# Optimization experiments

Hardware: AMD Instinct MI355X
Metric: run time of the kernel (lower is better)

The kernel has to match this reference:

```python
import jax, jax.numpy as jnp
import numpy as np

B, IN, H, Z = 2048, 1024, 1024, 256


def setup_inputs() -> dict:
    key = jax.random.key(0)
    ks = jax.random.split(key, 17)
    s = 1.0 / np.sqrt(H)  # matches reset_parameters uniform(-stdv, stdv)
    u = lambda k, shape: jax.random.uniform(k, shape, minval=-s, maxval=s, dtype=jnp.float32)
    return {
        'src_x': jax.random.normal(ks[0], (B, IN), dtype=jnp.float32),
        'h': jax.random.normal(ks[1], (B, H), dtype=jnp.float32),
        'c': jax.random.normal(ks[2], (B, H), dtype=jnp.float32),
        'src_meta': jax.random.normal(ks[3], (B, Z), dtype=jnp.float32),
        'zh_w': u(ks[4], (4 * Z, Z)),
        'zh_b': u(ks[5], (4 * Z,)),
        'zx_w': u(ks[6], (4 * Z, Z)),
        'zx_b': u(ks[7], (4 * Z,)),
        'zb_w': u(ks[8], (4 * Z, Z)),
        'dh_w': u(ks[9], (4, H, Z)),
        'dx_w': u(ks[10], (4, H, Z)),
        'db_w': u(ks[11], (4, H, Z)),
        'db_b': u(ks[12], (4, H)),
        'w_h': u(ks[13], (4, H, H)),
        'w_x': u(ks[14], (4, H, IN)),
        'ln_w': u(ks[15], (4, H)),
        'ln_b': u(ks[16], (4, H)),
    }


def reference(src_x, h, c, src_meta, zh_w, zh_b, zx_w, zx_b, zb_w,
              dh_w, dx_w, db_w, db_b, w_h, w_x, ln_w, ln_b):
    b = src_x.shape[0]
    # hypernetwork projections, reshaped to [B, 4 gates, Z]
    zh = (src_meta @ zh_w.T + zh_b).reshape(b, 4, -1)
    zx = (src_meta @ zx_w.T + zx_b).reshape(b, 4, -1)
    zb = (src_meta @ zb_w.T).reshape(b, 4, -1)
    # per-gate scaling vectors d_h, d_x and bias d_b: [B, 4, H]
    d_h = jnp.einsum('bgz,ghz->bgh', zh, dh_w)
    d_x = jnp.einsum('bgz,ghz->bgh', zx, dx_w)
    d_b = jnp.einsum('bgz,ghz->bgh', zb, db_w) + db_b[None]
    # main LSTM matmuls: [B, 4, H]
    wh = jnp.einsum('ghj,bj->bgh', w_h, h)
    wx = jnp.einsum('ghj,bj->bgh', w_x, src_x)
    y = d_h * wh + d_x * wx + d_b
    # per-gate LayerNorm over hidden dim (eps = 1e-5, torch default)
    mu = jnp.mean(y, axis=-1, keepdims=True)
    var = jnp.var(y, axis=-1, keepdims=True)
    yn = (y - mu) * jax.lax.rsqrt(var + 1e-5) * ln_w[None] + ln_b[None]
    i, f, g, o = yn[:, 0], yn[:, 1], yn[:, 2], yn[:, 3]
    c_next = jax.nn.sigmoid(f) * c + jax.nn.sigmoid(i) * jnp.tanh(g)
    h_next = jax.nn.sigmoid(o) * jnp.tanh(c_next)
    return (h_next, c_next)
```

## Files before the change

### kernel.cpp

```cpp
#include <hip/hip_runtime.h>

typedef __attribute__((ext_vector_type(4))) float f32x4;
typedef __attribute__((ext_vector_type(8))) short bf16x8;

#define DEVFN static __device__ __forceinline__

DEVFN unsigned short f2bf(float f) {
  union { float f; unsigned u; } x; x.f = f;
  unsigned r = x.u + 0x7fffu + ((x.u >> 16) & 1u);
  return (unsigned short)(r >> 16);
}
DEVFN float bf2f(unsigned short u) {
  union { unsigned u; float f; } x; x.u = ((unsigned)u) << 16;
  return x.f;
}

DEVFN void gload_lds16(const unsigned short* g, unsigned short* l) {
  __builtin_amdgcn_global_load_lds(
      (const __attribute__((address_space(1))) unsigned int*)g,
      (__attribute__((address_space(3))) unsigned int*)l, 16, 0, 0);
}

#define NSEG 8
struct SegTable {
  const float* src[NSEG];
  unsigned short* dst[NSEG];
  int chunks[NSEG];
};

__global__ __launch_bounds__(256) void prep_kernel(
    SegTable st, int castChunks,
    const float* __restrict__ zh_w, const float* __restrict__ zx_w,
    const float* __restrict__ zb_w, unsigned short* __restrict__ WzT,
    const float* __restrict__ zh_b, const float* __restrict__ zx_b,
    const float* __restrict__ db_b, const float* __restrict__ dh_w,
    const float* __restrict__ dx_w, float* __restrict__ F) {
  __shared__ float T[64][65];
  const int tid = threadIdx.x;
  int b = blockIdx.x;

  if (b < castChunks) {
    int c = b, s = 0;
    while (c >= st.chunks[s]) { c -= st.chunks[s]; ++s; }
    const float* src = st.src[s] + (long)c * 4096;
    unsigned short* dst = st.dst[s] + (long)c * 4096;
#pragma unroll
    for (int i = 0; i < 4; ++i) {
      float4 v = *(const float4*)(src + tid * 4 + i * 1024);
      ushort4 o;
      o.x = f2bf(v.x); o.y = f2bf(v.y); o.z = f2bf(v.z); o.w = f2bf(v.w);
      *(ushort4*)(dst + tid * 4 + i * 1024) = o;
    }
    return;
  }
  b -= castChunks;

  if (b < 192) {
    const int zz = b >> 4, rem = b & 15;
    const int t = zz >> 2, g = zz & 3;
    const float* src =
        (t == 0 ? zh_w : (t == 1 ? zx_w : zb_w)) + (long)g * 65536;
    unsigned short* dst = WzT + (long)zz * 65536;
    const int j0 = (rem & 3) * 64, k0 = (rem >> 2) * 64;
    const int jr = tid >> 2, kc = (tid & 3) * 16;
#pragma unroll
    for (int i = 0; i < 4; ++i) {
      float4 v = *(const float4*)(src + (long)(j0 + jr) * 256 + k0 + kc + i * 4);
      T[jr][kc + i * 4 + 0] = v.x;
      T[jr][kc + i * 4 + 1] = v.y;
      T[jr][kc + i * 4 + 2] = v.z;
      T[jr][kc + i * 4 + 3] = v.w;
    }
    __syncthreads();
    const int kr = tid >> 2, jc = (tid & 3) * 16;
    unsigned short tmp[16];
#pragma unroll
    for (int i = 0; i < 16; ++i) tmp[i] = f2bf(T[jc + i][kr]);
    *(bf16x8*)(dst + (long)(k0 + kr) * 256 + j0 + jc) = *(bf16x8*)&tmp[0];
    *(bf16x8*)(dst + (long)(k0 + kr) * 256 + j0 + jc + 8) = *(bf16x8*)&tmp[8];
    return;
  }
  b -= 192;

  if (b >= 128) {
    const int idx = (b - 128) * 1024 + tid * 4;
    *(float4*)(F + 8192 + idx) = *(const float4*)(db_b + idx);
    return;
  }
  const int wgid = b * 4 + (tid >> 6);
  const int lane = tid & 63;
  const int t = wgid >> 8, g = (wgid >> 6) & 3, hbase = (wgid & 63) * 16;
  const float* zb = (t == 0 ? zh_b : zx_b) + g * 256;
  const float* dw = (t == 0 ? dh_w : dx_w) + (long)g * 262144;
  float4 zv = *(const float4*)(zb + lane * 4);
#pragma unroll
  for (int i = 0; i < 16; ++i) {
    const int h = hbase + i;
    float4 wv = *(const float4*)(dw + (long)h * 256 + lane * 4);
    float s = zv.x * wv.x + zv.y * wv.y + zv.z * wv.z + zv.w * wv.w;
#pragma unroll
    for (int off = 32; off; off >>= 1) s += __shfl_down(s, off);
    if (lane == 0) F[(t * 4 + g) * 1024 + h] = s;
  }
}

DEVFN void gemm128_body(const unsigned short* __restrict__ A,
                        const unsigned short* __restrict__ W,
                        unsigned short* __restrict__ C,
                        const float* __restrict__ bias,
                        int lda, int ldb, int ldc, int K,
                        int bx, int by,
                        unsigned short* As, unsigned short* Bs) {
  const int m0 = by * 128, n0 = bx * 128;
  const int tid = threadIdx.x;
  const int lane = tid & 63, wid = tid >> 6;
  const int wr = wid >> 1, wc = wid & 1;

  const int srow = tid >> 2, scol = (tid & 3) * 8;
  const unsigned short* Ag0 = A + (long)(m0 + srow) * lda + scol;
  const unsigned short* Ag1 = A + (long)(m0 + 64 + srow) * lda + scol;
  const unsigned short* Wg0 = W + (long)(n0 + srow) * ldb + scol;
  const unsigned short* Wg1 = W + (long)(n0 + 64 + srow) * ldb + scol;
  unsigned short* As0 = &As[tid * 8];
  unsigned short* As1 = &As[2048 + tid * 8];
  unsigned short* Bs0 = &Bs[tid * 8];
  unsigned short* Bs1 = &Bs[2048 + tid * 8];

  const int r = lane & 15, q = lane >> 4;

  f32x4 acc[4][4];
#pragma unroll
  for (int m = 0; m < 4; ++m)
#pragma unroll
    for (int n = 0; n < 4; ++n) acc[m][n] = (f32x4)0.f;

  for (int k0 = 0; k0 < K; k0 += 32) {
    gload_lds16(Ag0 + k0, As0);
    gload_lds16(Ag1 + k0, As1);
    gload_lds16(Wg0 + k0, Bs0);
    gload_lds16(Wg1 + k0, Bs1);
    __syncthreads();

    bf16x8 af[4], bfr[4];
#pragma unroll
    for (int m = 0; m < 4; ++m)
      af[m] = *(const bf16x8*)&As[(wr * 64 + m * 16 + r) * 32 + q * 8];
#pragma unroll
    for (int n = 0; n < 4; ++n)
      bfr[n] = *(const bf16x8*)&Bs[(wc * 64 + n * 16 + r) * 32 + q * 8];
#pragma unroll
    for (int m = 0; m < 4; ++m)
#pragma unroll
      for (int n = 0; n < 4; ++n)
        acc[m][n] = __builtin_amdgcn_mfma_f32_16x16x32_bf16(af[m], bfr[n],
                                                            acc[m][n], 0, 0, 0);
    __syncthreads();
  }

#pragma unroll
  for (int m = 0; m < 4; ++m) {
    const int row = m0 + wr * 64 + m * 16 + q * 4;
#pragma unroll
    for (int n = 0; n < 4; ++n) {
      const int col = n0 + wc * 64 + n * 16 + r;
      float bv = bias ? bias[col] : 0.f;
#pragma unroll
      for (int j = 0; j < 4; ++j) {
        float v = acc[m][n][j] + bv;
        C[(long)(row + j) * ldc + col] = f2bf(v);
      }
    }
  }
}

__global__ __launch_bounds__(256) void gemm_e(
    const unsigned short* __restrict__ Wd, const unsigned short* __restrict__ WzT,
    unsigned short* __restrict__ E) {
  __shared__ __align__(16) unsigned short As[4096];
  __shared__ __align__(16) unsigned short Bs[4096];
  const int zz = blockIdx.z;
  gemm128_body(Wd + (long)zz * 262144, WzT + (long)zz * 65536,
               E + (long)zz * 262144, nullptr,
               256, 256, 256, 256, blockIdx.x, blockIdx.y, As, Bs);
}

__global__ __launch_bounds__(256) void gemm_d(
    const unsigned short* __restrict__ meta_bf, const unsigned short* __restrict__ E,
    unsigned short* __restrict__ dall, const float* __restrict__ F) {
  __shared__ __align__(16) unsigned short As[4096];
  __shared__ __align__(16) unsigned short Bs[4096];
  const int zz = blockIdx.z;
  unsigned short* C = dall + (long)(zz >> 2) * 8388608 + (zz & 3) * 1024;
  gemm128_body(meta_bf, E + (long)zz * 262144, C, F + zz * 1024,
               256, 256, 4096, 256, blockIdx.x, blockIdx.y, As, Bs);
}

__global__ __launch_bounds__(512, 2) void gemm256_whx(
    const unsigned short* __restrict__ Aall,
    const unsigned short* __restrict__ Ball,
    unsigned short* __restrict__ Call) {
  __shared__ __align__(16) unsigned short As[2][2][8192];
  __shared__ __align__(16) unsigned short Bs[2][2][8192];

  const int bid = blockIdx.x;
  const int swz = (bid & 7) * 32 + (bid >> 3);
  const int z = swz >> 7;
  const int rr = swz & 127;
  const int sb = rr >> 5, wq = rr & 31;
  const int my = (sb & 1) * 4 + (wq >> 3);
  const int nx = (sb >> 1) * 8 + (wq & 7);

  const unsigned short* Ag = Aall + (long)z * 2097152 + (long)my * 262144;
  const unsigned short* Bg = Ball + (long)z * 4194304 + (long)nx * 262144;
  unsigned short* Cg = Call + (long)z * 8388608 + (long)my * 1048576 + nx * 256;

  const int tid = threadIdx.x;
  const int lane = tid & 63, wid = tid >> 6;
  const int wm = wid >> 2, wn = wid & 3;
  const int fr = lane & 15, fq = lane >> 4;
  const int s0 = fq ^ (fr & 7);

  const int srow = tid >> 3, sslot = tid & 7;
  const int gcol = (sslot ^ (srow & 7)) * 8;
  const unsigned short* AgS = Ag + (long)srow * 1024 + gcol;
  const unsigned short* BgS = Bg + (long)srow * 1024 + gcol;

  auto stageA = [&](int buf, int half, int kt) {
    const unsigned short* s = AgS + half * 131072 + kt * 64;
    unsigned short* d = &As[buf][half][tid * 8];
    gload_lds16(s, d);
    gload_lds16(s + 65536, d + 4096);
  };
  auto stageB = [&](int buf, int half, int kt) {
    const unsigned short* s = BgS + half * 131072 + kt * 64;
    unsigned short* d = &Bs[buf][half][tid * 8];
    gload_lds16(s, d);
    gload_lds16(s + 65536, d + 4096);
  };

  int aoff[4], boff[2];
#pragma unroll
  for (int mf = 0; mf < 4; ++mf)
    aoff[mf] = (wm * 64 + mf * 16 + fr) * 64 + s0 * 8;
#pragma unroll
  for (int nf = 0; nf < 2; ++nf)
    boff[nf] = (wn * 32 + nf * 16 + fr) * 64 + s0 * 8;

  f32x4 acc[2][2][4][2];
#pragma unroll
  for (int i = 0; i < 2; ++i)
#pragma unroll
    for (int j = 0; j < 2; ++j)
#pragma unroll
      for (int m = 0; m < 4; ++m)
#pragma unroll
        for (int n = 0; n < 2; ++n) acc[i][j][m][n] = (f32x4)0.f;

  stageA(0, 0, 0); stageA(0, 1, 0); stageB(0, 0, 0); stageB(0, 1, 0);
  stageA(1, 0, 1); stageB(1, 0, 1); stageB(1, 1, 1);
  asm volatile("s_waitcnt vmcnt(6)" ::: "memory");
  __builtin_amdgcn_s_barrier();

  bf16x8 af[4][2], bA[2][2], bB[2][2];

#define PH_SYNC                                          \
  __builtin_amdgcn_s_barrier();                          \
  asm volatile("s_waitcnt lgkmcnt(0)" ::: "memory");     \
  __builtin_amdgcn_sched_barrier(0);

#define PH_MFMA(MH, NH, BR)                              \
  __builtin_amdgcn_s_setprio(1);                         \
  _Pragma("unroll")                                      \
  for (int mf = 0; mf < 4; ++mf)                         \
    _Pragma("unroll")                                    \
    for (int nf = 0; nf < 2; ++nf) {                     \
      acc[MH][NH][mf][nf] = __builtin_amdgcn_mfma_f32_16x16x32_bf16( \
          af[mf][0], BR[nf][0], acc[MH][NH][mf][nf], 0, 0, 0);       \
      acc[MH][NH][mf][nf] = __builtin_amdgcn_mfma_f32_16x16x32_bf16( \
          af[mf][1], BR[nf][1], acc[MH][NH][mf][nf], 0, 0, 0);       \
    }                                                    \
  __builtin_amdgcn_s_setprio(0);

#pragma unroll 2
  for (int T = 0; T < 16; ++T) {
    const int buf = T & 1, nb = buf ^ 1;

    {
      const unsigned short* Ab = &As[buf][0][0];
      const unsigned short* Bb = &Bs[buf][0][0];
#pragma unroll
      for (int mf = 0; mf < 4; ++mf) {
        af[mf][0] = *(const bf16x8*)(Ab + aoff[mf]);
        af[mf][1] = *(const bf16x8*)(Ab + (aoff[mf] ^ 32));
      }
#pragma unroll
      for (int nf = 0; nf < 2; ++nf) {
        bA[nf][0] = *(const bf16x8*)(Bb + boff[nf]);
        bA[nf][1] = *(const bf16x8*)(Bb + (boff[nf] ^ 32));
      }
      if (T < 15) stageA(nb, 1, T + 1);
      PH_SYNC;
      PH_MFMA(0, 0, bA);
      __builtin_amdgcn_s_barrier();
    }
    {
      const unsigned short* Bb = &Bs[buf][1][0];
#pragma unroll
      for (int nf = 0; nf < 2; ++nf) {
        bB[nf][0] = *(const bf16x8*)(Bb + boff[nf]);
        bB[nf][1] = *(const bf16x8*)(Bb + (boff[nf] ^ 32));
      }
      if (T < 14) stageA(buf, 0, T + 2);
      PH_SYNC;
      PH_MFMA(0, 1, bB);
      __builtin_amdgcn_s_barrier();
    }
    {
      const unsigned short* Ab = &As[buf][1][0];
#pragma unroll
      for (int mf = 0; mf < 4; ++mf) {
        af[mf][0] = *(const bf16x8*)(Ab + aoff[mf]);
        af[mf][1] = *(const bf16x8*)(Ab + (aoff[mf] ^ 32));
      }
      if (T < 14) { stageB(buf, 0, T + 2); stageB(buf, 1, T + 2); }
      PH_SYNC;
      PH_MFMA(1, 0, bA);
      PH_MFMA(1, 1, bB);
      if (T < 14) {
        asm volatile("s_waitcnt vmcnt(6)" ::: "memory");
      } else if (T == 14) {
        asm volatile("s_waitcnt vmcnt(0)" ::: "memory");
      }
      __builtin_amdgcn_s_barrier();
    }
  }
#undef PH_SYNC
#undef PH_MFMA

#pragma unroll
  for (int mh = 0; mh < 2; ++mh)
#pragma unroll
    for (int nh = 0; nh < 2; ++nh)
#pragma unroll
      for (int mf = 0; mf < 4; ++mf)
#pragma unroll
        for (int nf = 0; nf < 2; ++nf) {
          const int row = mh * 128 + wm * 64 + mf * 16 + fq * 4;
          const int col = nh * 128 + wn * 32 + nf * 16 + fr;
#pragma unroll
          for (int j = 0; j < 4; ++j)
            Cg[(long)(row + j) * 4096 + col] = f2bf(acc[mh][nh][mf][nf][j]);
        }
}

DEVFN void ld4bf(const unsigned short* p, float* o) {
  ushort4 v = *(const ushort4*)p;
  o[0] = bf2f(v.x); o[1] = bf2f(v.y); o[2] = bf2f(v.z); o[3] = bf2f(v.w);
}

__global__ __launch_bounds__(256) void epilogue_kernel(
    const unsigned short* __restrict__ d_all,
    const unsigned short* __restrict__ whx,
    const float* __restrict__ c_in,
    const float* __restrict__ ln_w, const float* __restrict__ ln_b,
    float* __restrict__ out) {
  const long b = blockIdx.x;
  const int t = threadIdx.x;
  const int lane = t & 63, wid = t >> 6;

  const unsigned short* dh = d_all + b * 4096;
  const unsigned short* dx = d_all + 8388608L + b * 4096;
  const unsigned short* db = d_all + 16777216L + b * 4096;
  const unsigned short* wh = whx + b * 4096;
  const unsigned short* wx = whx + 8388608L + b * 4096;

  __shared__ float redS[4][4], redQ[4][4];
  float y[4][4];

#pragma unroll
  for (int g = 0; g < 4; ++g) {
    const int base = g * 1024 + t * 4;
    float fdh[4], fdx[4], fdb[4], fwh[4], fwx[4];
    ld4bf(dh + base, fdh);
    ld4bf(dx + base, fdx);
    ld4bf(db + base, fdb);
    ld4bf(wh + base, fwh);
    ld4bf(wx + base, fwx);
    float s = 0.f, sq = 0.f;
#pragma unroll
    for (int j = 0; j < 4; ++j) {
      float v = fdh[j] * fwh[j] + fdx[j] * fwx[j] + fdb[j];
      y[g][j] = v;
      s += v;
      sq += v * v;
    }
#pragma unroll
    for (int off = 32; off; off >>= 1) {
      s += __shfl_down(s, off);
      sq += __shfl_down(sq, off);
    }
    if (lane == 0) { redS[g][wid] = s; redQ[g][wid] = sq; }
  }
  __syncthreads();

  float yn[4][4];
#pragma unroll
  for (int g = 0; g < 4; ++g) {
    float S = redS[g][0] + redS[g][1] + redS[g][2] + redS[g][3];
    float SQ = redQ[g][0] + redQ[g][1] + redQ[g][2] + redQ[g][3];
    float mu = S * (1.f / 1024.f);
    float var = SQ * (1.f / 1024.f) - mu * mu;
    float rs = rsqrtf(var + 1e-5f);
    const int base = g * 1024 + t * 4;
    float4 lw = *(const float4*)(ln_w + base);
    float4 lb = *(const float4*)(ln_b + base);
    yn[g][0] = (y[g][0] - mu) * rs * lw.x + lb.x;
    yn[g][1] = (y[g][1] - mu) * rs * lw.y + lb.y;
    yn[g][2] = (y[g][2] - mu) * rs * lw.z + lb.z;
    yn[g][3] = (y[g][3] - mu) * rs * lw.w + lb.w;
  }

  float4 cp = *(const float4*)(c_in + b * 1024 + t * 4);
  float cin[4] = {cp.x, cp.y, cp.z, cp.w};
  float hn[4], cn[4];
#pragma unroll
  for (int j = 0; j < 4; ++j) {
    float ii = yn[0][j], ff = yn[1][j], gg = yn[2][j], oo = yn[3][j];
    float si = 1.f / (1.f + expf(-ii));
    float sf = 1.f / (1.f + expf(-ff));
    float so = 1.f / (1.f + expf(-oo));
    float cnj = sf * cin[j] + si * tanhf(gg);
    cn[j] = cnj;
    hn[j] = so * tanhf(cnj);
  }
  float4 ho = {hn[0], hn[1], hn[2], hn[3]};
  float4 co = {cn[0], cn[1], cn[2], cn[3]};
  *(float4*)(out + b * 1024 + t * 4) = ho;
  *(float4*)(out + 2097152L + b * 1024 + t * 4) = co;
}

extern "C" void kernel_launch(void* const* d_in, const int* in_sizes, int n_in,
                              void* d_out, int out_size, void* d_ws,
                              size_t ws_size, hipStream_t stream) {
  const float* src_x = (const float*)d_in[0];
  const float* h_in  = (const float*)d_in[1];
  const float* c_in  = (const float*)d_in[2];
  const float* meta  = (const float*)d_in[3];
  const float* zh_w  = (const float*)d_in[4];
  const float* zh_b  = (const float*)d_in[5];
  const float* zx_w  = (const float*)d_in[6];
  const float* zx_b  = (const float*)d_in[7];
  const float* zb_w  = (const float*)d_in[8];
  const float* dh_w  = (const float*)d_in[9];
  const float* dx_w  = (const float*)d_in[10];
  const float* db_w  = (const float*)d_in[11];
  const float* db_b  = (const float*)d_in[12];
  const float* w_h   = (const float*)d_in[13];
  const float* w_x   = (const float*)d_in[14];
  const float* ln_w  = (const float*)d_in[15];
  const float* ln_b  = (const float*)d_in[16];

  char* ws = (char*)d_ws;
  unsigned short* h_bf    = (unsigned short*)(ws + 0);
  unsigned short* x_bf    = (unsigned short*)(ws + 4194304);
  unsigned short* meta_bf = (unsigned short*)(ws + 8388608);
  unsigned short* Wh      = (unsigned short*)(ws + 9437184);
  unsigned short* Wx      = (unsigned short*)(ws + 17825792);
  unsigned short* Wd      = (unsigned short*)(ws + 26214400);
  unsigned short* WzT     = (unsigned short*)(ws + 32505856);
  unsigned short* E       = (unsigned short*)(ws + 34078720);
  float*          F       = (float*)(ws + 40370176);
  unsigned short* dall    = (unsigned short*)(ws + 40419328);
  unsigned short* whx     = (unsigned short*)(ws + 90750976);
  if (ws_size < 124305408) return;

  SegTable st;
  int i = 0, total = 0;
  auto add = [&](const float* s, unsigned short* d, int n) {
    st.src[i] = s; st.dst[i] = d; st.chunks[i] = n / 4096;
    total += n / 4096; ++i;
  };
  add(h_in, h_bf, 2048 * 1024);
  add(src_x, x_bf, 2048 * 1024);
  add(meta, meta_bf, 2048 * 256);
  add(w_h, Wh, 4096 * 1024);
  add(w_x, Wx, 4096 * 1024);
  add(dh_w, Wd, 4 * 1024 * 256);
  add(dx_w, Wd + 1048576, 4 * 1024 * 256);
  add(db_w, Wd + 2097152, 4 * 1024 * 256);

  prep_kernel<<<total + 192 + 132, 256, 0, stream>>>(
      st, total, zh_w, zx_w, zb_w, WzT, zh_b, zx_b, db_b, dh_w, dx_w, F);

  gemm_e<<<dim3(2, 8, 12), 256, 0, stream>>>(Wd, WzT, E);

  gemm_d<<<dim3(8, 16, 12), 256, 0, stream>>>(meta_bf, E, dall, F);

  gemm256_whx<<<256, 512, 0, stream>>>(h_bf, Wh, whx);

  epilogue_kernel<<<2048, 256, 0, stream>>>(dall, whx, c_in, ln_w, ln_b,
                                            (float*)d_out);
}
```

Measured before the change: 115.5 us.

## Shrink whx GEMM tile to 256x128, single-buffer B, double grid for occupancy

The main h/x GEMM moves from 256x256 output tiles with double-buffered A and B in LDS to 256x128 tiles with a single B buffer and an A split across two halves. This cuts LDS and accumulator registers per block, so launch bounds can ask for 4 blocks per CU, and the grid grows to 512 blocks to fill the GPU. The cost is less reuse of A per tile, which means more global traffic. The pipeline also gets shallower, with full vmcnt(0) waits each phase, so load latency is less hidden.

```diff
diff --git a/kernel.cpp b/kernel.cpp
--- a/kernel.cpp
+++ b/kernel.cpp
@@ -195,24 +195,24 @@
                256, 256, 4096, 256, blockIdx.x, blockIdx.y, As, Bs);
 }
 
-__global__ __launch_bounds__(512, 2) void gemm256_whx(
+__global__ __launch_bounds__(512, 4) void gemm256_whx(
     const unsigned short* __restrict__ Aall,
     const unsigned short* __restrict__ Ball,
     unsigned short* __restrict__ Call) {
-  __shared__ __align__(16) unsigned short As[2][2][8192];
-  __shared__ __align__(16) unsigned short Bs[2][2][8192];
+  __shared__ __align__(16) unsigned short As[2][8192];
+  __shared__ __align__(16) unsigned short Bs[8192];
 
   const int bid = blockIdx.x;
-  const int swz = (bid & 7) * 32 + (bid >> 3);
-  const int z = swz >> 7;
-  const int rr = swz & 127;
-  const int sb = rr >> 5, wq = rr & 31;
-  const int my = (sb & 1) * 4 + (wq >> 3);
-  const int nx = (sb >> 1) * 8 + (wq & 7);
+  const int swz = (bid & 7) * 64 + (bid >> 3);
+  const int z = swz >> 8;
+  const int rr = swz & 255;
+  const int sb = rr >> 6, wq = rr & 63;
+  const int my = wq >> 3;
+  const int nx = sb * 8 + (wq & 7);
 
   const unsigned short* Ag = Aall + (long)z * 2097152 + (long)my * 262144;
-  const unsigned short* Bg = Ball + (long)z * 4194304 + (long)nx * 262144;
-  unsigned short* Cg = Call + (long)z * 8388608 + (long)my * 1048576 + nx * 256;
+  const unsigned short* Bg = Ball + (long)z * 4194304 + (long)nx * 131072;
+  unsigned short* Cg = Call + (long)z * 8388608 + (long)my * 1048576 + nx * 128;
 
   const int tid = threadIdx.x;
   const int lane = tid & 63, wid = tid >> 6;
@@ -225,15 +225,15 @@
   const unsigned short* AgS = Ag + (long)srow * 1024 + gcol;
   const unsigned short* BgS = Bg + (long)srow * 1024 + gcol;
 
-  auto stageA = [&](int buf, int half, int kt) {
+  auto stageA = [&](int half, int kt) {
     const unsigned short* s = AgS + half * 131072 + kt * 64;
-    unsigned short* d = &As[buf][half][tid * 8];
+    unsigned short* d = &As[half][tid * 8];
     gload_lds16(s, d);
     gload_lds16(s + 65536, d + 4096);
   };
-  auto stageB = [&](int buf, int half, int kt) {
-    const unsigned short* s = BgS + half * 131072 + kt * 64;
-    unsigned short* d = &Bs[buf][half][tid * 8];
+  auto stageB = [&](int kt) {
+    const unsigned short* s = BgS + kt * 64;
+    unsigned short* d = &Bs[tid * 8];
     gload_lds16(s, d);
     gload_lds16(s + 65536, d + 4096);
   };
@@ -246,48 +246,43 @@
   for (int nf = 0; nf < 2; ++nf)
     boff[nf] = (wn * 32 + nf * 16 + fr) * 64 + s0 * 8;
 
-  f32x4 acc[2][2][4][2];
+  f32x4 acc[2][4][2];
 #pragma unroll
   for (int i = 0; i < 2; ++i)
 #pragma unroll
-    for (int j = 0; j < 2; ++j)
-#pragma unroll
-      for (int m = 0; m < 4; ++m)
-#pragma unroll
-        for (int n = 0; n < 2; ++n) acc[i][j][m][n] = (f32x4)0.f;
-
-  stageA(0, 0, 0); stageA(0, 1, 0); stageB(0, 0, 0); stageB(0, 1, 0);
-  stageA(1, 0, 1); stageB(1, 0, 1); stageB(1, 1, 1);
-  asm volatile("s_waitcnt vmcnt(6)" ::: "memory");
+    for (int m = 0; m < 4; ++m)
+#pragma unroll
+      for (int n = 0; n < 2; ++n) acc[i][m][n] = (f32x4)0.f;
+
+  stageA(0, 0); stageB(0); stageA(1, 0);
+  asm volatile("s_waitcnt vmcnt(2)" ::: "memory");
   __builtin_amdgcn_s_barrier();
 
-  bf16x8 af[4][2], bA[2][2], bB[2][2];
+  bf16x8 af[4][2], bfr[2][2];
 
 #define PH_SYNC                                          \
   __builtin_amdgcn_s_barrier();                          \
   asm volatile("s_waitcnt lgkmcnt(0)" ::: "memory");     \
   __builtin_amdgcn_sched_barrier(0);
 
-#define PH_MFMA(MH, NH, BR)                              \
+#define PH_MFMA(MH)                                      \
   __builtin_amdgcn_s_setprio(1);                         \
   _Pragma("unroll")                                      \
   for (int mf = 0; mf < 4; ++mf)                         \
     _Pragma("unroll")                                    \
     for (int nf = 0; nf < 2; ++nf) {                     \
-      acc[MH][NH][mf][nf] = __builtin_amdgcn_mfma_f32_16x16x32_bf16( \
-          af[mf][0], BR[nf][0], acc[MH][NH][mf][nf], 0, 0, 0);       \
-      acc[MH][NH][mf][nf] = __builtin_amdgcn_mfma_f32_16x16x32_bf16( \
-          af[mf][1], BR[nf][1], acc[MH][NH][mf][nf], 0, 0, 0);       \
+      acc[MH][mf][nf] = __builtin_amdgcn_mfma_f32_16x16x32_bf16( \
+          af[mf][0], bfr[nf][0], acc[MH][mf][nf], 0, 0, 0);      \
+      acc[MH][mf][nf] = __builtin_amdgcn_mfma_f32_16x16x32_bf16( \
+          af[mf][1], bfr[nf][1], acc[MH][mf][nf], 0, 0, 0);      \
     }                                                    \
   __builtin_amdgcn_s_setprio(0);
 
 #pragma unroll 2
   for (int T = 0; T < 16; ++T) {
-    const int buf = T & 1, nb = buf ^ 1;
-
     {
-      const unsigned short* Ab = &As[buf][0][0];
-      const unsigned short* Bb = &Bs[buf][0][0];
+      if (T >= 1) stageA(1, T);
+      const unsigned short* Ab = &As[0][0];
 #pragma unroll
       for (int mf = 0; mf < 4; ++mf) {
         af[mf][0] = *(const bf16x8*)(Ab + aoff[mf]);
@@ -295,40 +290,25 @@
       }
 #pragma unroll
       for (int nf = 0; nf < 2; ++nf) {
-        bA[nf][0] = *(const bf16x8*)(Bb + boff[nf]);
-        bA[nf][1] = *(const bf16x8*)(Bb + (boff[nf] ^ 32));
-      }
-      if (T < 15) stageA(nb, 1, T + 1);
+        bfr[nf][0] = *(const bf16x8*)(Bs + boff[nf]);
+        bfr[nf][1] = *(const bf16x8*)(Bs + (boff[nf] ^ 32));
+      }
       PH_SYNC;
-      PH_MFMA(0, 0, bA);
+      PH_MFMA(0);
+      asm volatile("s_waitcnt vmcnt(0)" ::: "memory");
       __builtin_amdgcn_s_barrier();
     }
     {
-      const unsigned short* Bb = &Bs[buf][1][0];
-#pragma unroll
-      for (int nf = 0; nf < 2; ++nf) {
-        bB[nf][0] = *(const bf16x8*)(Bb + boff[nf]);
-        bB[nf][1] = *(const bf16x8*)(Bb + (boff[nf] ^ 32));
-      }
-      if (T < 14) stageA(buf, 0, T + 2);
-      PH_SYNC;
-      PH_MFMA(0, 1, bB);
-      __builtin_amdgcn_s_barrier();
-    }
-    {
-      const unsigned short* Ab = &As[buf][1][0];
+      if (T < 15) { stageA(0, T + 1); stageB(T + 1); }
+      const unsigned short* Ab = &As[1][0];
 #pragma unroll
       for (int mf = 0; mf < 4; ++mf) {
         af[mf][0] = *(const bf16x8*)(Ab + aoff[mf]);
         af[mf][1] = *(const bf16x8*)(Ab + (aoff[mf] ^ 32));
       }
-      if (T < 14) { stageB(buf, 0, T + 2); stageB(buf, 1, T + 2); }
       PH_SYNC;
-      PH_MFMA(1, 0, bA);
-      PH_MFMA(1, 1, bB);
-      if (T < 14) {
-        asm volatile("s_waitcnt vmcnt(6)" ::: "memory");
-      } else if (T == 14) {
+      PH_MFMA(1);
+      if (T < 15) {
         asm volatile("s_waitcnt vmcnt(0)" ::: "memory");
       }
       __builtin_amdgcn_s_barrier();
@@ -340,17 +320,15 @@
 #pragma unroll
   for (int mh = 0; mh < 2; ++mh)
 #pragma unroll
-    for (int nh = 0; nh < 2; ++nh)
-#pragma unroll
-      for (int mf = 0; mf < 4; ++mf)
-#pragma unroll
-        for (int nf = 0; nf < 2; ++nf) {
-          const int row = mh * 128 + wm * 64 + mf * 16 + fq * 4;
-          const int col = nh * 128 + wn * 32 + nf * 16 + fr;
-#pragma unroll
-          for (int j = 0; j < 4; ++j)
-            Cg[(long)(row + j) * 4096 + col] = f2bf(acc[mh][nh][mf][nf][j]);
-        }
+    for (int mf = 0; mf < 4; ++mf)
+#pragma unroll
+      for (int nf = 0; nf < 2; ++nf) {
+        const int row = mh * 128 + wm * 64 + mf * 16 + fq * 4;
+        const int col = wn * 32 + nf * 16 + fr;
+#pragma unroll
+        for (int j = 0; j < 4; ++j)
+          Cg[(long)(row + j) * 4096 + col] = f2bf(acc[mh][mf][nf][j]);
+      }
 }
 
 DEVFN void ld4bf(const unsigned short* p, float* o) {
@@ -496,7 +474,7 @@
 
   gemm_d<<<dim3(8, 16, 12), 256, 0, stream>>>(meta_bf, E, dall, F);
 
-  gemm256_whx<<<256, 512, 0, stream>>>(h_bf, Wh, whx);
+  gemm256_whx<<<512, 512, 0, stream>>>(h_bf, Wh, whx);
 
   epilogue_kernel<<<2048, 256, 0, stream>>>(dall, whx, c_in, ln_w, ln_b,
                                             (float*)d_out);
```

Result: no change. 117.3 us (+1.6%).
